# Performance work log

Measured on AMD Instinct MI355X. Metric: run time of the kernel, lower is better.

## Reference

```python
import jax, jax.numpy as jnp
import numpy as np


def conv2d(x, w, b=None):
    # NCHW conv, stride 1, 'same' padding inferred from kernel size
    ph, pw = w.shape[2] // 2, w.shape[3] // 2
    y = jax.lax.conv_general_dilated(
        x, w, window_strides=(1, 1), padding=[(ph, ph), (pw, pw)],
        dimension_numbers=('NCHW', 'OIHW', 'NCHW'))
    if b is not None:
        y = y + b[None, :, None, None]
    return y


def gelu(v):
    return jax.nn.gelu(v, approximate=False)  # torch nn.GELU default (erf)


def lrelu(v):
    return jnp.where(v >= 0, v, 0.1 * v)  # LeakyReLU(0.1)


def setup_inputs() -> dict:
    key = jax.random.key(0)
    ks = jax.random.split(key, 16)
    B, C, H, W = 2, 32, 256, 256
    s = 0.05
    return {
        'x':      jax.random.normal(ks[0], (B, C, H, W), jnp.float32),
        'key':    jax.random.normal(ks[1], (B, C, H, W), jnp.float32),
        'w_off1': jax.random.normal(ks[2], (32, 64, 3, 3), jnp.float32) * s,
        'b_off1': jax.random.normal(ks[3], (32,), jnp.float32) * s,
        'w_off2': jax.random.normal(ks[4], (32, 32, 3, 3), jnp.float32) * s,
        'b_off2': jax.random.normal(ks[5], (32,), jnp.float32) * s,
        'w_dcn':  jax.random.normal(ks[6], (288, 64, 3, 3), jnp.float32) * s,
        'b_dcn':  jax.random.normal(ks[7], (288,), jnp.float32) * s,
        'w_sel':  jax.random.normal(ks[8], (1, 3, 3, 3), jnp.float32) * s,
        'b_sel':  jax.random.normal(ks[9], (1,), jnp.float32) * s,
        'w_t1':   jax.random.normal(ks[10], (32, 32, 3, 3), jnp.float32) * s,
        'w_t2':   jax.random.normal(ks[11], (128, 32, 1, 1), jnp.float32) * s,
        'w_t3':   jax.random.normal(ks[12], (128, 128, 3, 3), jnp.float32) * s,
        'w_t4':   jax.random.normal(ks[13], (32, 128, 1, 1), jnp.float32) * s,
        'w_t5':   jax.random.normal(ks[14], (32, 32, 3, 3), jnp.float32) * s,
    }


def reference(x, key, w_off1, b_off1, w_off2, b_off2, w_dcn, b_dcn,
              w_sel, b_sel, w_t1, w_t2, w_t3, w_t4, w_t5):
    B, C, H, W = x.shape
    TOPK = 3
    # offset branch
    off = lrelu(conv2d(jnp.concatenate([x, key], axis=1), w_off1, b_off1))
    off = lrelu(conv2d(off, w_off2, b_off2))
    # dcn_attention proxy: conv over (key, offset) producing C*9 candidate warps
    warp = conv2d(jnp.concatenate([key, off], axis=1), w_dcn, b_dcn)
    warp = warp.reshape(B, C, 9, H, W)
    # correlation of each of 9 candidates with x, per pixel
    corr = jnp.einsum('bcohw,bchw->bohw', warp, x)            # [B,9,H,W]
    corr = corr.reshape(B, 9, H * W).transpose(0, 2, 1)       # [B,HW,9]
    _, idx = jax.lax.top_k(corr, TOPK)                        # [B,HW,3]
    # gather selected candidates per pixel per channel
    warp_p = warp.reshape(B, C, 9, H * W).transpose(0, 3, 2, 1)   # [B,HW,9,C]
    sel = jnp.take_along_axis(warp_p, idx[..., None], axis=2)     # [B,HW,3,C]
    key_warp = sel.reshape(B, H, W, TOPK, C).transpose(0, 4, 3, 1, 2)
    key_warp = key_warp.reshape(B * C, TOPK, H, W)
    key_warp = conv2d(key_warp, w_sel, b_sel).reshape(B, C, H, W)
    # tail: conv-GELU bottleneck stack
    y = conv2d(key_warp, w_t1)
    y = conv2d(gelu(y), w_t2)
    y = conv2d(gelu(y), w_t3)
    y = conv2d(gelu(y), w_t4)
    y = conv2d(gelu(y), w_t5)
    return y
```

## Files before the change

### kernel.cpp

```cpp
#include <hip/hip_runtime.h>
#include <math.h>

static constexpr int H = 256, W = 256, HW = H * W;

typedef __attribute__((ext_vector_type(8))) _Float16 half8v;
typedef __attribute__((ext_vector_type(4))) _Float16 half4v;
typedef __attribute__((ext_vector_type(4))) float  float4v;

__device__ __forceinline__ half8v h8zero() {
  half8v z;
  #pragma unroll
  for (int i = 0; i < 8; ++i) z[i] = (_Float16)0;
  return z;
}

__device__ __forceinline__ float gelu_f(float v) {
  return 0.5f * v * (1.0f + erff(v * 0.70710678118654752440f));
}
template<int ACT>
__device__ __forceinline__ float apply_act(float v) {
  if constexpr (ACT == 1) return v >= 0.f ? v : 0.1f * v;
  if constexpr (ACT == 2) return gelu_f(v);
  return v;
}

__global__ __launch_bounds__(256)
void pack2_k(const float* __restrict__ inA, _Float16* __restrict__ hiA, _Float16* __restrict__ loA,
             const float* __restrict__ inB, _Float16* __restrict__ hiB, _Float16* __restrict__ loB)
{
  const int p = blockIdx.x * 256 + threadIdx.x;
  const int b = blockIdx.y;
  const float* in = blockIdx.z ? inB : inA;
  _Float16* hi = blockIdx.z ? hiB : hiA;
  _Float16* lo = blockIdx.z ? loB : loA;
  const float* ip = in + (size_t)b * 32 * HW + p;
  __attribute__((aligned(16))) _Float16 hv[32], lv[32];
  #pragma unroll
  for (int c = 0; c < 32; ++c) {
    float v = ip[(size_t)c * HW];
    _Float16 h = (_Float16)v;
    hv[c] = h;
    lv[c] = (_Float16)((v - (float)h) * 2048.0f);
  }
  size_t ob = ((size_t)b * HW + p) * 32;
  #pragma unroll
  for (int j = 0; j < 4; ++j) {
    *(half8v*)&hi[ob + j * 8] = *(half8v*)&hv[j * 8];
    *(half8v*)&lo[ob + j * 8] = *(half8v*)&lv[j * 8];
  }
}

__device__ __forceinline__ void prep_w_body(const float* w, _Float16* hi, _Float16* lo,
                                            int OC, int CIN, int tid)
{
  if (tid >= OC * CIN * 9) return;
  int ci = tid % CIN; int r = tid / CIN; int oc = r % OC; int tap = r / OC;
  float v = w[((size_t)oc * CIN + ci) * 9 + tap];
  _Float16 h = (_Float16)v;
  hi[tid] = h;
  lo[tid] = (_Float16)((v - (float)h) * 2048.0f);
}
__global__ __launch_bounds__(256)
void prep3_w_k(const float* __restrict__ w0, _Float16* __restrict__ h0, _Float16* __restrict__ l0, int OC0, int CIN0, int nb0,
               const float* __restrict__ w1, _Float16* __restrict__ h1, _Float16* __restrict__ l1, int OC1, int CIN1, int nb1,
               const float* __restrict__ w2, _Float16* __restrict__ h2, _Float16* __restrict__ l2, int OC2, int CIN2)
{
  int bb = blockIdx.x;
  if (bb < nb0)            prep_w_body(w0, h0, l0, OC0, CIN0, bb * 256 + threadIdx.x);
  else if (bb < nb0 + nb1) prep_w_body(w1, h1, l1, OC1, CIN1, (bb - nb0) * 256 + threadIdx.x);
  else                     prep_w_body(w2, h2, l2, OC2, CIN2, (bb - nb0 - nb1) * 256 + threadIdx.x);
}

template<int CIN, int OC, int OCB, int ACT, int OMODE, int SPLIT>
__global__ __launch_bounds__(256)
void conv3x3_mfma_k(const _Float16* __restrict__ iH0, const _Float16* __restrict__ iL0,
                    const _Float16* __restrict__ iH1, const _Float16* __restrict__ iL1, int cin0,
                    const _Float16* __restrict__ wHi, const _Float16* __restrict__ wLo,
                    const float* __restrict__ bias,
                    float* __restrict__ outF, _Float16* __restrict__ oH, _Float16* __restrict__ oL)
{
  constexpr int NOF  = OCB / 16;
  constexpr int nOcg = OC / OCB;
  __shared__ _Float16 sB[6 * 66 * 32];

  const int l  = threadIdx.x & 63;
  const int wv = threadIdx.x >> 6;

  const int bid = blockIdx.x;
  const int xcd = bid & 7, q = bid >> 3;
  const int ocg  = q % nOcg;
  const int tIdx = (q / nOcg) * 8 + xcd;
  const int b   = tIdx >> 8;
  const int x0  = ((tIdx >> 6) & 3) * 64;
  const int y0  = (tIdx & 63) * 4;
  const int oc0 = ocg * OCB;

  float4v accP[NOF][4];
  float4v accQ[(SPLIT == 3) ? NOF : 1][4];
  #pragma unroll
  for (int j = 0; j < NOF; ++j)
    #pragma unroll
    for (int f = 0; f < 4; ++f) {
      accP[j][f] = (float4v){0.f, 0.f, 0.f, 0.f};
      if constexpr (SPLIT == 3) accQ[j][f] = (float4v){0.f, 0.f, 0.f, 0.f};
    }

  const int k8  = (l >> 4) * 8;
  const int ocl = l & 15;
  const int rowy = y0 + wv;
  const int sq  = l & 3;
  const int spx = l >> 2;

  #pragma unroll 1
  for (int cc = 0; cc < CIN; cc += 32) {
    const _Float16 *cbH, *cbL;
    if (cc < cin0) {
      size_t o = (size_t)(b * (cin0 >> 5) + (cc >> 5)) * HW * 32;
      cbH = iH0 + o; cbL = iL0 + o;
    } else {
      size_t o = (size_t)(b * ((CIN - cin0) >> 5) + ((cc - cin0) >> 5)) * HW * 32;
      cbH = iH1 + o; cbL = iL1 + o;
    }
    __syncthreads();
    #pragma unroll 2
    for (int t = wv; t < 30; t += 4) {
      int r = t / 5; int s = t - r * 5;
      int gy = y0 + r - 1;
      bool vy = (gy >= 0) && (gy < H);
      int gyc = gy < 0 ? 0 : (gy >= H ? H - 1 : gy);
      int pxl = s * 16 + spx;
      bool lact = (s < 4) || (l < 8);
      int gx = x0 + pxl - 1;
      bool vx = (gx >= 0) && (gx < W);
      int gxc = gx < 0 ? 0 : (gx >= W ? W - 1 : gx);
      half8v v = h8zero();
      if (lact && vy && vx)
        v = *(const half8v*)&cbH[((size_t)gyc * W + gxc) * 32 + sq * 8];
      int cls = (sq ^ pxl) & 3;
      if (lact)
        *(half8v*)&sB[(r * 66 + pxl) * 32 + cls * 8] = v;
    }
    __syncthreads();

    #pragma unroll 1
    for (int tap = 0; tap < 9; ++tap) {
      const int dy = tap / 3, dx = tap - 3 * dy;
      const int gy = rowy + dy - 1;
      const bool vy = (gy >= 0) && (gy < H);
      const int gyc = gy < 0 ? 0 : (gy >= H ? H - 1 : gy);
      const size_t rowb = (size_t)gyc * W;

      half8v bq[(SPLIT == 3) ? 4 : 1];
      if constexpr (SPLIT == 3) {
        #pragma unroll
        for (int f = 0; f < 4; ++f) {
          int gx = x0 + f * 16 + ocl + dx - 1;
          bool ok = vy && ((unsigned)gx < (unsigned)W);
          int gxc = gx < 0 ? 0 : (gx >= W ? W - 1 : gx);
          half8v vl = *(const half8v*)&cbL[(rowb + gxc) * 32 + k8];
          bq[f] = ok ? vl : h8zero();
        }
      }
      half8v ah[NOF], aq[(SPLIT == 3) ? NOF : 1];
      const _Float16* hp = wHi + ((size_t)tap * OC + oc0 + ocl) * CIN + cc + k8;
      #pragma unroll
      for (int j = 0; j < NOF; ++j)
        ah[j] = *(const half8v*)(hp + (size_t)j * 16 * CIN);
      if constexpr (SPLIT == 3) {
        const _Float16* lp = wLo + ((size_t)tap * OC + oc0 + ocl) * CIN + cc + k8;
        #pragma unroll
        for (int j = 0; j < NOF; ++j)
          aq[j] = *(const half8v*)(lp + (size_t)j * 16 * CIN);
      }
      const int px = ocl + dx;
      const int rbase = ((wv + dy) * 66 + px) * 32;
      const int clsH = ((l >> 4) ^ px) & 3;
      #pragma unroll
      for (int f = 0; f < 4; ++f) {
        half8v bh = *(const half8v*)&sB[rbase + f * 512 + clsH * 8];
        #pragma unroll
        for (int j = 0; j < NOF; ++j) {
          accP[j][f] = __builtin_amdgcn_mfma_f32_16x16x32_f16(ah[j], bh, accP[j][f], 0, 0, 0);
          if constexpr (SPLIT == 3) {
            accQ[j][f] = __builtin_amdgcn_mfma_f32_16x16x32_f16(ah[j], bq[f], accQ[j][f], 0, 0, 0);
            accQ[j][f] = __builtin_amdgcn_mfma_f32_16x16x32_f16(aq[j], bh, accQ[j][f], 0, 0, 0);
          }
        }
      }
    }
  }

  #pragma unroll
  for (int j = 0; j < NOF; ++j)
    #pragma unroll
    for (int f = 0; f < 4; ++f) {
      const int px  = x0 + f * 16 + ocl;
      const int occ = oc0 + j * 16 + (l >> 4) * 4;
      float vv4[4];
      #pragma unroll
      for (int r = 0; r < 4; ++r) {
        float bv = bias ? bias[occ + r] : 0.f;
        float vv = accP[j][f][r] + bv;
        if constexpr (SPLIT == 3) vv += accQ[j][f][r] * (1.0f / 2048.0f);
        vv4[r] = apply_act<ACT>(vv);
      }
      if constexpr (OMODE == 0) {
        #pragma unroll
        for (int r = 0; r < 4; ++r)
          outF[((size_t)(b * OC + occ + r) * H + rowy) * W + px] = vv4[r];
      } else if constexpr (OMODE == 1) {
        __attribute__((aligned(8))) _Float16 hv[4], lv[4];
        #pragma unroll
        for (int r = 0; r < 4; ++r) {
          _Float16 h = (_Float16)vv4[r];
          hv[r] = h;
          lv[r] = (_Float16)((vv4[r] - (float)h) * 2048.0f);
        }
        size_t ob = ((size_t)b * HW + (size_t)rowy * W + px) * OC + occ;
        *(half4v*)&oH[ob] = *(half4v*)&hv[0];
        *(half4v*)&oL[ob] = *(half4v*)&lv[0];
      } else {
        float4 v4;
        v4.x = vv4[0]; v4.y = vv4[1]; v4.z = vv4[2]; v4.w = vv4[3];
        *(float4*)&outF[((size_t)b * HW + (size_t)rowy * W + px) * OC + occ] = v4;
      }
    }
}

template<int CIN, int OCB, int ACT>
__global__ __launch_bounds__(256)
void conv1x1_nhwc_k(const float* __restrict__ in, const float* __restrict__ w,
                    _Float16* __restrict__ oH, int OC)
{
  __shared__ __align__(16) float sW[OCB][CIN];
  const int b   = blockIdx.y;
  const int oc0 = blockIdx.z * OCB;
  for (int t = threadIdx.x; t < OCB * CIN; t += 256)
    sW[t / CIN][t % CIN] = w[(size_t)(oc0 + t / CIN) * CIN + (t % CIN)];
  __syncthreads();

  const int pb = blockIdx.x * 1024 + threadIdx.x;
  float acc[OCB][4];
  #pragma unroll
  for (int o = 0; o < OCB; ++o)
    #pragma unroll
    for (int i = 0; i < 4; ++i) acc[o][i] = 0.f;

  #pragma unroll 1
  for (int c0 = 0; c0 < CIN; c0 += 8) {
    float v[4][8];
    #pragma unroll
    for (int i = 0; i < 4; ++i) {
      const float* ip = in + ((size_t)b * HW + pb + i * 256) * CIN + c0;
      float4 a = *(const float4*)ip;
      float4 c = *(const float4*)(ip + 4);
      v[i][0]=a.x; v[i][1]=a.y; v[i][2]=a.z; v[i][3]=a.w;
      v[i][4]=c.x; v[i][5]=c.y; v[i][6]=c.z; v[i][7]=c.w;
    }
    #pragma unroll
    for (int o = 0; o < OCB; ++o) {
      const float4 w0 = *(const float4*)&sW[o][c0];
      const float4 w1 = *(const float4*)&sW[o][c0 + 4];
      #pragma unroll
      for (int i = 0; i < 4; ++i) {
        acc[o][i] += v[i][0]*w0.x + v[i][1]*w0.y + v[i][2]*w0.z + v[i][3]*w0.w
                   + v[i][4]*w1.x + v[i][5]*w1.y + v[i][6]*w1.z + v[i][7]*w1.w;
      }
    }
  }
  #pragma unroll
  for (int i = 0; i < 4; ++i) {
    __attribute__((aligned(16))) _Float16 hv[OCB];
    #pragma unroll
    for (int o = 0; o < OCB; ++o)
      hv[o] = (_Float16)apply_act<ACT>(acc[o][i]);
    size_t ob = ((size_t)(b * (OC >> 5) + (oc0 >> 5)) * HW + pb + i * 256) * 32 + (oc0 & 31);
    #pragma unroll
    for (int j = 0; j < OCB / 8; ++j)
      *(half8v*)&oH[ob + j * 8] = *(half8v*)&hv[j * 8];
  }
}

__global__ __launch_bounds__(256)
void corr_topk_k(const float* __restrict__ warp, const float* __restrict__ x,
                 int* __restrict__ idxo)
{
  const int p = blockIdx.x * 256 + threadIdx.x;
  const int b = blockIdx.y;
  float corr[9];
  #pragma unroll
  for (int o = 0; o < 9; ++o) corr[o] = 0.f;
  #pragma unroll 2
  for (int c = 0; c < 32; ++c) {
    float xv = x[((size_t)b * 32 + c) * HW + p];
    const float* wp = warp + ((size_t)b * 288 + (size_t)c * 9) * HW + p;
    #pragma unroll
    for (int o = 0; o < 9; ++o) corr[o] += wp[(size_t)o * HW] * xv;
  }
  unsigned mask = 0;
  int packed = 0;
  #pragma unroll
  for (int t = 0; t < 3; ++t) {
    float best = -INFINITY; int bi = 0;
    #pragma unroll
    for (int o = 0; o < 9; ++o) {
      bool take = (((mask >> o) & 1u) == 0u) && (corr[o] > best);
      best = take ? corr[o] : best;
      bi   = take ? o       : bi;
    }
    mask   |= 1u << bi;
    packed |= bi << (4 * t);
  }
  idxo[(size_t)b * HW + p] = packed;
}

__global__ __launch_bounds__(256)
void selconv_k(const float* __restrict__ warp, const int* __restrict__ idxp,
               const float* __restrict__ wsel, const float* __restrict__ bsel,
               _Float16* __restrict__ oH)
{
  const int tx = threadIdx.x & 31, ty = threadIdx.x >> 5;
  const int px = blockIdx.x * 32 + tx;
  const int py = blockIdx.y * 8 + ty;
  const int b  = blockIdx.z;

  int  nidx[9];
  bool nval[9];
  int  qoff[9];
  #pragma unroll
  for (int kh = 0; kh < 3; ++kh)
    #pragma unroll
    for (int kw = 0; kw < 3; ++kw) {
      int k = kh * 3 + kw;
      int qy = py + kh - 1, qx = px + kw - 1;
      nval[k] = (qy >= 0 && qy < H && qx >= 0 && qx < W);
      qoff[k] = qy * W + qx;
      nidx[k] = nval[k] ? idxp[(size_t)b * HW + qoff[k]] : 0;
    }

  float ws27[27];
  #pragma unroll
  for (int i = 0; i < 27; ++i) ws27[i] = wsel[i];
  const float bs = bsel[0];

  float arr[32];
  #pragma unroll 1
  for (int c = 0; c < 32; ++c) {
    float acc = bs;
    const float* wb = warp + ((size_t)b * 288 + (size_t)c * 9) * HW;
    #pragma unroll
    for (int k = 0; k < 9; ++k) {
      if (nval[k]) {
        int pk = nidx[k];
        #pragma unroll
        for (int t = 0; t < 3; ++t) {
          int o = (pk >> (4 * t)) & 15;
          acc += ws27[t * 9 + k] * wb[(size_t)o * HW + qoff[k]];
        }
      }
    }
    arr[c] = acc;
  }

  __attribute__((aligned(16))) _Float16 hv[32];
  #pragma unroll
  for (int c = 0; c < 32; ++c) hv[c] = (_Float16)arr[c];
  size_t ob = ((size_t)b * HW + (size_t)py * W + px) * 32;
  #pragma unroll
  for (int j = 0; j < 4; ++j)
    *(half8v*)&oH[ob + j * 8] = *(half8v*)&hv[j * 8];
}

extern "C" void kernel_launch(void* const* d_in, const int* in_sizes, int n_in,
                              void* d_out, int out_size, void* d_ws, size_t ws_size,
                              hipStream_t stream) {
  const float* x      = (const float*)d_in[0];
  const float* key    = (const float*)d_in[1];
  const float* w_off1 = (const float*)d_in[2];
  const float* b_off1 = (const float*)d_in[3];
  const float* w_off2 = (const float*)d_in[4];
  const float* b_off2 = (const float*)d_in[5];
  const float* w_dcn  = (const float*)d_in[6];
  const float* b_dcn  = (const float*)d_in[7];
  const float* w_sel  = (const float*)d_in[8];
  const float* b_sel  = (const float*)d_in[9];
  const float* w_t1   = (const float*)d_in[10];
  const float* w_t2   = (const float*)d_in[11];
  const float* w_t3   = (const float*)d_in[12];
  const float* w_t4   = (const float*)d_in[13];
  const float* w_t5   = (const float*)d_in[14];

  char* ws = (char*)d_ws;
  float* warp = (float*)(ws);
  _Float16* xH  = (_Float16*)(ws);
  _Float16* xL  = (_Float16*)(ws + 8388608);
  _Float16* o1H = (_Float16*)(ws + 16777216);
  _Float16* o1L = (_Float16*)(ws + 25165824);
  _Float16* w1H = (_Float16*)(ws + 33554432);
  _Float16* w1L = w1H + 18432;
  _Float16* w2H = w1L + 18432;
  _Float16* w2L = w2H + 9216;
  _Float16* kH  = (_Float16*)(ws + 150994944);
  _Float16* kL  = (_Float16*)(ws + 159383552);
  _Float16* o2H = (_Float16*)(ws + 167772160);
  _Float16* o2L = (_Float16*)(ws + 176160768);
  _Float16* wdH = (_Float16*)(ws + 184549376);
  _Float16* wdL = wdH + 165888;
  int*      idxb = (int*)(ws + 150994944);
  _Float16* kwH  = (_Float16*)(ws + 159383552);
  _Float16* twB  = (_Float16*)(ws + 176160768);
  _Float16* t1H_w = twB;
  _Float16* t1L_w = twB + 9216;
  _Float16* t3H_w = twB + 18432;
  _Float16* t3L_w = twB + 165888;
  _Float16* t5H_w = twB + 313344;
  _Float16* t5L_w = twB + 322560;
  float*    y1  = (float*)(ws);
  _Float16* t2H = (_Float16*)(ws + 16777216);
  float*    y3  = (float*)(ws + 83886080);
  _Float16* t4H = (_Float16*)(ws + 50331648);
  float* out = (float*)d_out;

  dim3 blk(256);

  pack2_k<<<dim3(256, 2, 2), blk, 0, stream>>>(x, xH, xL, key, kH, kL);
  prep3_w_k<<<dim3(756), blk, 0, stream>>>(
      w_off1, w1H, w1L, 32, 64, 72,
      w_off2, w2H, w2L, 32, 32, 36,
      w_dcn,  wdH, wdL, 288, 64);

  conv3x3_mfma_k<64, 32, 32, 1, 1, 3><<<dim3(512), blk, 0, stream>>>(
      xH, xL, kH, kL, 32, w1H, w1L, b_off1, nullptr, o1H, o1L);
  conv3x3_mfma_k<32, 32, 32, 1, 1, 3><<<dim3(512), blk, 0, stream>>>(
      o1H, o1L, o1H, o1L, 32, w2H, w2L, b_off2, nullptr, o2H, o2L);
  conv3x3_mfma_k<64, 288, 48, 0, 0, 3><<<dim3(3072), blk, 0, stream>>>(
      kH, kL, o2H, o2L, 32, wdH, wdL, b_dcn, warp, nullptr, nullptr);
  corr_topk_k<<<dim3(256, 2), blk, 0, stream>>>(warp, x, idxb);
  selconv_k<<<dim3(8, 32, 2), blk, 0, stream>>>(warp, idxb, w_sel, b_sel, kwH);

  prep3_w_k<<<dim3(648), blk, 0, stream>>>(
      w_t1, t1H_w, t1L_w, 32, 32, 36,
      w_t3, t3H_w, t3L_w, 128, 128, 576,
      w_t5, t5H_w, t5L_w, 32, 32);

  conv3x3_mfma_k<32, 32, 32, 2, 2, 1><<<dim3(512), blk, 0, stream>>>(
      kwH, kwH, kwH, kwH, 32, t1H_w, t1L_w, nullptr, y1, nullptr, nullptr);
  conv1x1_nhwc_k<32, 16, 2><<<dim3(64, 2, 8), blk, 0, stream>>>(y1, w_t2, t2H, 128);
  conv3x3_mfma_k<128, 128, 64, 2, 2, 1><<<dim3(1024), blk, 0, stream>>>(
      t2H, t2H, t2H, t2H, 128, t3H_w, t3L_w, nullptr, y3, nullptr, nullptr);
  conv1x1_nhwc_k<128, 16, 2><<<dim3(64, 2, 2), blk, 0, stream>>>(y3, w_t4, t4H, 32);
  conv3x3_mfma_k<32, 32, 32, 0, 0, 1><<<dim3(512), blk, 0, stream>>>(
      t4H, t4H, t4H, t4H, 32, t5H_w, t5L_w, nullptr, out, nullptr, nullptr);
}
```

Measured before the change: 725.8 us.

## Double-buffer per-tap weight and low-half loads in conv3x3 MFMA kernel

```diff
diff --git a/kernel.cpp b/kernel.cpp
--- a/kernel.cpp
+++ b/kernel.cpp
@@ -80,6 +80,8 @@
                     float* __restrict__ outF, _Float16* __restrict__ oH, _Float16* __restrict__ oL)
 {
   constexpr int NOF  = OCB / 16;
+  constexpr int NBQ  = (SPLIT == 3) ? 4 : 1;
+  constexpr int NAQ  = (SPLIT == 3) ? NOF : 1;
   constexpr int nOcg = OC / OCB;
   __shared__ _Float16 sB[6 * 66 * 32];
 
@@ -96,14 +98,17 @@
   const int oc0 = ocg * OCB;
 
   float4v accP[NOF][4];
-  float4v accQ[(SPLIT == 3) ? NOF : 1][4];
+  float4v accQ[NAQ][4];
   #pragma unroll
   for (int j = 0; j < NOF; ++j)
     #pragma unroll
-    for (int f = 0; f < 4; ++f) {
+    for (int f = 0; f < 4; ++f)
       accP[j][f] = (float4v){0.f, 0.f, 0.f, 0.f};
-      if constexpr (SPLIT == 3) accQ[j][f] = (float4v){0.f, 0.f, 0.f, 0.f};
-    }
+  #pragma unroll
+  for (int j = 0; j < NAQ; ++j)
+    #pragma unroll
+    for (int f = 0; f < 4; ++f)
+      accQ[j][f] = (float4v){0.f, 0.f, 0.f, 0.f};
 
   const int k8  = (l >> 4) * 8;
   const int ocl = l & 15;
@@ -140,28 +145,25 @@
       if (lact)
         *(half8v*)&sB[(r * 66 + pxl) * 32 + cls * 8] = v;
     }
-    __syncthreads();
-
-    #pragma unroll 1
-    for (int tap = 0; tap < 9; ++tap) {
-      const int dy = tap / 3, dx = tap - 3 * dy;
-      const int gy = rowy + dy - 1;
-      const bool vy = (gy >= 0) && (gy < H);
-      const int gyc = gy < 0 ? 0 : (gy >= H ? H - 1 : gy);
-      const size_t rowb = (size_t)gyc * W;
-
-      half8v bq[(SPLIT == 3) ? 4 : 1];
+
+    half8v bqA[NBQ], ahA[NOF], aqA[NAQ];
+    half8v bqB[NBQ], ahB[NOF], aqB[NAQ];
+
+    auto LOADG = [&](int tap, half8v (&bq)[NBQ], half8v (&ah)[NOF], half8v (&aq)[NAQ]) {
+      const int dy = tap / 3, dx = tap - 3 * (tap / 3);
       if constexpr (SPLIT == 3) {
+        const int gy = rowy + dy - 1;
+        const bool vy = (gy >= 0) && (gy < H);
+        const int gyc = gy < 0 ? 0 : (gy >= H ? H - 1 : gy);
         #pragma unroll
         for (int f = 0; f < 4; ++f) {
           int gx = x0 + f * 16 + ocl + dx - 1;
           bool ok = vy && ((unsigned)gx < (unsigned)W);
           int gxc = gx < 0 ? 0 : (gx >= W ? W - 1 : gx);
-          half8v vl = *(const half8v*)&cbL[(rowb + gxc) * 32 + k8];
+          half8v vl = *(const half8v*)&cbL[((size_t)gyc * W + gxc) * 32 + k8];
           bq[f] = ok ? vl : h8zero();
         }
       }
-      half8v ah[NOF], aq[(SPLIT == 3) ? NOF : 1];
       const _Float16* hp = wHi + ((size_t)tap * OC + oc0 + ocl) * CIN + cc + k8;
       #pragma unroll
       for (int j = 0; j < NOF; ++j)
@@ -172,6 +174,9 @@
         for (int j = 0; j < NOF; ++j)
           aq[j] = *(const half8v*)(lp + (size_t)j * 16 * CIN);
       }
+    };
+    auto COMPUTE = [&](int tap, half8v (&bq)[NBQ], half8v (&ah)[NOF], half8v (&aq)[NAQ]) {
+      const int dy = tap / 3, dx = tap - 3 * (tap / 3);
       const int px = ocl + dx;
       const int rbase = ((wv + dy) * 66 + px) * 32;
       const int clsH = ((l >> 4) ^ px) & 3;
@@ -187,7 +192,18 @@
           }
         }
       }
-    }
+    };
+
+    LOADG(0, bqA, ahA, aqA);
+    __syncthreads();
+    #pragma unroll
+    for (int tp = 0; tp < 4; ++tp) {
+      LOADG(2 * tp + 1, bqB, ahB, aqB);
+      COMPUTE(2 * tp, bqA, ahA, aqA);
+      LOADG(2 * tp + 2, bqA, ahA, aqA);
+      COMPUTE(2 * tp + 1, bqB, ahB, aqB);
+    }
+    COMPUTE(8, bqA, ahA, aqA);
   }
 
   #pragma unroll
@@ -433,7 +449,7 @@
       xH, xL, kH, kL, 32, w1H, w1L, b_off1, nullptr, o1H, o1L);
   conv3x3_mfma_k<32, 32, 32, 1, 1, 3><<<dim3(512), blk, 0, stream>>>(
       o1H, o1L, o1H, o1L, 32, w2H, w2L, b_off2, nullptr, o2H, o2L);
-  conv3x3_mfma_k<64, 288, 48, 0, 0, 3><<<dim3(3072), blk, 0, stream>>>(
+  conv3x3_mfma_k<64, 288, 32, 0, 0, 3><<<dim3(4608), blk, 0, stream>>>(
       kH, kL, o2H, o2L, 32, wdH, wdL, b_dcn, warp, nullptr, nullptr);
   corr_topk_k<<<dim3(256, 2), blk, 0, stream>>>(warp, x, idxb);
   selconv_k<<<dim3(8, 32, 2), blk, 0, stream>>>(warp, idxb, w_sel, b_sel, kwH);
```

Measured after the change: 727.1 us. No clear change (+0.2%).

## Halve conv spatial tile width and stage low-half inputs in shared memory

Applied to the files above, without the earlier changes.

```diff
diff --git a/kernel.cpp b/kernel.cpp
--- a/kernel.cpp
+++ b/kernel.cpp
@@ -80,8 +80,10 @@
                     float* __restrict__ outF, _Float16* __restrict__ oH, _Float16* __restrict__ oL)
 {
   constexpr int NOF  = OCB / 16;
+  constexpr int NAQ  = (SPLIT == 3) ? NOF : 1;
+  constexpr int REC  = (SPLIT == 3) ? 64 : 32;
   constexpr int nOcg = OC / OCB;
-  __shared__ _Float16 sB[6 * 66 * 32];
+  __shared__ _Float16 sB[6 * 34 * REC];
 
   const int l  = threadIdx.x & 63;
   const int wv = threadIdx.x >> 6;
@@ -90,20 +92,23 @@
   const int xcd = bid & 7, q = bid >> 3;
   const int ocg  = q % nOcg;
   const int tIdx = (q / nOcg) * 8 + xcd;
-  const int b   = tIdx >> 8;
-  const int x0  = ((tIdx >> 6) & 3) * 64;
+  const int b   = tIdx >> 9;
+  const int x0  = ((tIdx >> 6) & 7) * 32;
   const int y0  = (tIdx & 63) * 4;
   const int oc0 = ocg * OCB;
 
-  float4v accP[NOF][4];
-  float4v accQ[(SPLIT == 3) ? NOF : 1][4];
+  float4v accP[NOF][2];
+  float4v accQ[NAQ][2];
   #pragma unroll
   for (int j = 0; j < NOF; ++j)
     #pragma unroll
-    for (int f = 0; f < 4; ++f) {
+    for (int f = 0; f < 2; ++f)
       accP[j][f] = (float4v){0.f, 0.f, 0.f, 0.f};
-      if constexpr (SPLIT == 3) accQ[j][f] = (float4v){0.f, 0.f, 0.f, 0.f};
-    }
+  #pragma unroll
+  for (int j = 0; j < NAQ; ++j)
+    #pragma unroll
+    for (int f = 0; f < 2; ++f)
+      accQ[j][f] = (float4v){0.f, 0.f, 0.f, 0.f};
 
   const int k8  = (l >> 4) * 8;
   const int ocl = l & 15;
@@ -122,46 +127,52 @@
       cbH = iH1 + o; cbL = iL1 + o;
     }
     __syncthreads();
-    #pragma unroll 2
-    for (int t = wv; t < 30; t += 4) {
-      int r = t / 5; int s = t - r * 5;
-      int gy = y0 + r - 1;
-      bool vy = (gy >= 0) && (gy < H);
-      int gyc = gy < 0 ? 0 : (gy >= H ? H - 1 : gy);
-      int pxl = s * 16 + spx;
-      bool lact = (s < 4) || (l < 8);
-      int gx = x0 + pxl - 1;
-      bool vx = (gx >= 0) && (gx < W);
-      int gxc = gx < 0 ? 0 : (gx >= W ? W - 1 : gx);
-      half8v v = h8zero();
-      if (lact && vy && vx)
-        v = *(const half8v*)&cbH[((size_t)gyc * W + gxc) * 32 + sq * 8];
-      int cls = (sq ^ pxl) & 3;
-      if (lact)
-        *(half8v*)&sB[(r * 66 + pxl) * 32 + cls * 8] = v;
+    if constexpr (SPLIT == 3) {
+      #pragma unroll 2
+      for (int t = wv; t < 36; t += 4) {
+        int r = t / 6; int rem = t - r * 6; int bsel = rem / 3; int s = rem - bsel * 3;
+        const _Float16* src = bsel ? cbL : cbH;
+        int gy = y0 + r - 1;
+        bool vy = (gy >= 0) && (gy < H);
+        int gyc = gy < 0 ? 0 : (gy >= H ? H - 1 : gy);
+        int pxl = s * 16 + spx;
+        bool lact = (s < 2) || (l < 8);
+        int gx = x0 + pxl - 1;
+        bool vx = (gx >= 0) && (gx < W);
+        int gxc = gx < 0 ? 0 : (gx >= W ? W - 1 : gx);
+        half8v v = h8zero();
+        if (lact && vy && vx)
+          v = *(const half8v*)&src[((size_t)gyc * W + gxc) * 32 + sq * 8];
+        int cls = (sq + (bsel ? 4 : 0)) ^ (pxl & 7);
+        if (lact)
+          *(half8v*)&sB[(r * 34 + pxl) * 64 + cls * 8] = v;
+      }
+    } else {
+      #pragma unroll 2
+      for (int t = wv; t < 18; t += 4) {
+        int r = t / 3; int s = t - r * 3;
+        int gy = y0 + r - 1;
+        bool vy = (gy >= 0) && (gy < H);
+        int gyc = gy < 0 ? 0 : (gy >= H ? H - 1 : gy);
+        int pxl = s * 16 + spx;
+        bool lact = (s < 2) || (l < 8);
+        int gx = x0 + pxl - 1;
+        bool vx = (gx >= 0) && (gx < W);
+        int gxc = gx < 0 ? 0 : (gx >= W ? W - 1 : gx);
+        half8v v = h8zero();
+        if (lact && vy && vx)
+          v = *(const half8v*)&cbH[((size_t)gyc * W + gxc) * 32 + sq * 8];
+        int cls = (sq ^ pxl) & 3;
+        if (lact)
+          *(half8v*)&sB[(r * 34 + pxl) * 32 + cls * 8] = v;
+      }
     }
     __syncthreads();
 
     #pragma unroll 1
     for (int tap = 0; tap < 9; ++tap) {
-      const int dy = tap / 3, dx = tap - 3 * dy;
-      const int gy = rowy + dy - 1;
-      const bool vy = (gy >= 0) && (gy < H);
-      const int gyc = gy < 0 ? 0 : (gy >= H ? H - 1 : gy);
-      const size_t rowb = (size_t)gyc * W;
-
-      half8v bq[(SPLIT == 3) ? 4 : 1];
-      if constexpr (SPLIT == 3) {
-        #pragma unroll
-        for (int f = 0; f < 4; ++f) {
-          int gx = x0 + f * 16 + ocl + dx - 1;
-          bool ok = vy && ((unsigned)gx < (unsigned)W);
-          int gxc = gx < 0 ? 0 : (gx >= W ? W - 1 : gx);
-          half8v vl = *(const half8v*)&cbL[(rowb + gxc) * 32 + k8];
-          bq[f] = ok ? vl : h8zero();
-        }
-      }
-      half8v ah[NOF], aq[(SPLIT == 3) ? NOF : 1];
+      const int dy = tap / 3, dx = tap - 3 * (tap / 3);
+      half8v ah[NOF], aq[NAQ];
       const _Float16* hp = wHi + ((size_t)tap * OC + oc0 + ocl) * CIN + cc + k8;
       #pragma unroll
       for (int j = 0; j < NOF; ++j)
@@ -173,19 +184,31 @@
           aq[j] = *(const half8v*)(lp + (size_t)j * 16 * CIN);
       }
       const int px = ocl + dx;
-      const int rbase = ((wv + dy) * 66 + px) * 32;
-      const int clsH = ((l >> 4) ^ px) & 3;
-      #pragma unroll
-      for (int f = 0; f < 4; ++f) {
-        half8v bh = *(const half8v*)&sB[rbase + f * 512 + clsH * 8];
-        #pragma unroll
-        for (int j = 0; j < NOF; ++j) {
-          accP[j][f] = __builtin_amdgcn_mfma_f32_16x16x32_f16(ah[j], bh, accP[j][f], 0, 0, 0);
-          if constexpr (SPLIT == 3) {
-            accQ[j][f] = __builtin_amdgcn_mfma_f32_16x16x32_f16(ah[j], bq[f], accQ[j][f], 0, 0, 0);
+      if constexpr (SPLIT == 3) {
+        const int rbase = ((wv + dy) * 34 + px) * 64;
+        const int clsH = (l >> 4) ^ (px & 7);
+        const int clsQ = ((l >> 4) + 4) ^ (px & 7);
+        #pragma unroll
+        for (int f = 0; f < 2; ++f) {
+          half8v bh = *(const half8v*)&sB[rbase + f * 1024 + clsH * 8];
+          half8v bq = *(const half8v*)&sB[rbase + f * 1024 + clsQ * 8];
+          #pragma unroll
+          for (int j = 0; j < NOF; ++j) {
+            accP[j][f] = __builtin_amdgcn_mfma_f32_16x16x32_f16(ah[j], bh, accP[j][f], 0, 0, 0);
+            accQ[j][f] = __builtin_amdgcn_mfma_f32_16x16x32_f16(ah[j], bq, accQ[j][f], 0, 0, 0);
             accQ[j][f] = __builtin_amdgcn_mfma_f32_16x16x32_f16(aq[j], bh, accQ[j][f], 0, 0, 0);
           }
         }
+      } else {
+        const int rbase = ((wv + dy) * 34 + px) * 32;
+        const int clsH = ((l >> 4) ^ px) & 3;
+        #pragma unroll
+        for (int f = 0; f < 2; ++f) {
+          half8v bh = *(const half8v*)&sB[rbase + f * 512 + clsH * 8];
+          #pragma unroll
+          for (int j = 0; j < NOF; ++j)
+            accP[j][f] = __builtin_amdgcn_mfma_f32_16x16x32_f16(ah[j], bh, accP[j][f], 0, 0, 0);
+        }
       }
     }
   }
@@ -193,7 +216,7 @@
   #pragma unroll
   for (int j = 0; j < NOF; ++j)
     #pragma unroll
-    for (int f = 0; f < 4; ++f) {
+    for (int f = 0; f < 2; ++f) {
       const int px  = x0 + f * 16 + ocl;
       const int occ = oc0 + j * 16 + (l >> 4) * 4;
       float vv4[4];
@@ -429,11 +452,11 @@
       w_off2, w2H, w2L, 32, 32, 36,
       w_dcn,  wdH, wdL, 288, 64);
 
-  conv3x3_mfma_k<64, 32, 32, 1, 1, 3><<<dim3(512), blk, 0, stream>>>(
+  conv3x3_mfma_k<64, 32, 32, 1, 1, 3><<<dim3(1024), blk, 0, stream>>>(
       xH, xL, kH, kL, 32, w1H, w1L, b_off1, nullptr, o1H, o1L);
-  conv3x3_mfma_k<32, 32, 32, 1, 1, 3><<<dim3(512), blk, 0, stream>>>(
+  conv3x3_mfma_k<32, 32, 32, 1, 1, 3><<<dim3(1024), blk, 0, stream>>>(
       o1H, o1L, o1H, o1L, 32, w2H, w2L, b_off2, nullptr, o2H, o2L);
-  conv3x3_mfma_k<64, 288, 48, 0, 0, 3><<<dim3(3072), blk, 0, stream>>>(
+  conv3x3_mfma_k<64, 288, 32, 0, 0, 3><<<dim3(9216), blk, 0, stream>>>(
       kH, kL, o2H, o2L, 32, wdH, wdL, b_dcn, warp, nullptr, nullptr);
   corr_topk_k<<<dim3(256, 2), blk, 0, stream>>>(warp, x, idxb);
   selconv_k<<<dim3(8, 32, 2), blk, 0, stream>>>(warp, idxb, w_sel, b_sel, kwH);
@@ -443,12 +466,12 @@
       w_t3, t3H_w, t3L_w, 128, 128, 576,
       w_t5, t5H_w, t5L_w, 32, 32);
 
-  conv3x3_mfma_k<32, 32, 32, 2, 2, 1><<<dim3(512), blk, 0, stream>>>(
+  conv3x3_mfma_k<32, 32, 32, 2, 2, 1><<<dim3(1024), blk, 0, stream>>>(
       kwH, kwH, kwH, kwH, 32, t1H_w, t1L_w, nullptr, y1, nullptr, nullptr);
   conv1x1_nhwc_k<32, 16, 2><<<dim3(64, 2, 8), blk, 0, stream>>>(y1, w_t2, t2H, 128);
-  conv3x3_mfma_k<128, 128, 64, 2, 2, 1><<<dim3(1024), blk, 0, stream>>>(
+  conv3x3_mfma_k<128, 128, 64, 2, 2, 1><<<dim3(2048), blk, 0, stream>>>(
       t2H, t2H, t2H, t2H, 128, t3H_w, t3L_w, nullptr, y3, nullptr, nullptr);
   conv1x1_nhwc_k<128, 16, 2><<<dim3(64, 2, 2), blk, 0, stream>>>(y3, w_t4, t4H, 32);
-  conv3x3_mfma_k<32, 32, 32, 0, 0, 1><<<dim3(512), blk, 0, stream>>>(
+  conv3x3_mfma_k<32, 32, 32, 0, 0, 1><<<dim3(1024), blk, 0, stream>>>(
       t4H, t4H, t4H, t4H, 32, t5H_w, t5L_w, nullptr, out, nullptr, nullptr);
 }
```

New measurement: 860.7 us. +18.6%, slower.
